# Kernel tuning notes

Hardware: AMD Instinct MI355X
Metric: run time of the kernel (lower is better)

Reference implementation:

```python
import jax, jax.numpy as jnp
import numpy as np
import math

B, S, HID = 16, 512, 768
NUM_LABELS = 9
NUM_HEADS = 4
HEAD_DIM = HID // NUM_HEADS
MAX_REL = 5
B_PERSON = 1
I_PERSON = 2
LN_EPS = 1e-5


def setup_inputs() -> dict:
    key = jax.random.key(0)
    ks = jax.random.split(key, 16)
    w = lambda k, shp: jax.random.normal(k, shp, dtype=jnp.float32) * 0.02
    return {
        "sequence_output": jax.random.normal(ks[0], (B, S, HID), dtype=jnp.float32),
        "Wq": w(ks[1], (HID, HID)), "bq": jnp.zeros((HID,), jnp.float32),
        "Wk": w(ks[2], (HID, HID)), "bk": jnp.zeros((HID,), jnp.float32),
        "Wv": w(ks[3], (HID, HID)), "bv": jnp.zeros((HID,), jnp.float32),
        "Wo": w(ks[4], (HID, HID)), "bo": jnp.zeros((HID,), jnp.float32),
        "ln_g": jnp.ones((HID,), jnp.float32), "ln_b": jnp.zeros((HID,), jnp.float32),
        "Ws": w(ks[5], (HID, NUM_LABELS)), "bs": jnp.zeros((NUM_LABELS,), jnp.float32),
        "entity_bias": w(ks[6], (NUM_LABELS,)),
    }


def _heads(x):
    # [B,S,HID] -> [B,H,S,D]
    return x.reshape(B, S, NUM_HEADS, HEAD_DIM).transpose(0, 2, 1, 3)


def reference(sequence_output, Wq, bq, Wk, bk, Wv, bv, Wo, bo, ln_g, ln_b, Ws, bs, entity_bias):
    x = sequence_output
    q = _heads(x @ Wq + bq)
    k = _heads(x @ Wk + bk)
    v = _heads(x @ Wv + bv)

    scores = jnp.einsum("bhqd,bhkd->bhqk", q, k)
    # relative position bias: exp(-0.1 * clamp(|i-j|, 0, MAX_REL)), broadcast over b,h
    idx = jnp.arange(S, dtype=jnp.float32)
    dist = jnp.abs(idx[None, :] - idx[:, None])  # [S,S]
    rel_bias = jnp.exp(-0.1 * jnp.clip(dist, 0.0, float(MAX_REL)))
    dist_mask = -0.1 * dist
    scores = (scores + rel_bias) / math.sqrt(HEAD_DIM) + dist_mask
    probs = jax.nn.softmax(scores, axis=-1)  # dropout is identity in eval

    ctx = jnp.einsum("bhqk,bhkd->bhqd", probs, v)
    ctx = ctx.transpose(0, 2, 1, 3).reshape(B, S, HID)
    out = ctx @ Wo + bo

    h = x + out
    mu = jnp.mean(h, axis=-1, keepdims=True)
    var = jnp.mean(jnp.square(h - mu), axis=-1, keepdims=True)
    h = (h - mu) * jax.lax.rsqrt(var + LN_EPS) * ln_g + ln_b

    span_logits = h @ Ws + bs  # [B,S,L]
    # vectorized entity-bias post-process: the torch loop adds entity_bias[I_PERSON]
    # TWICE to final_logits[:, j, I_PERSON] whenever argmax(span_logits[:, j-1]) == B_PERSON
    prev_is_b = jnp.argmax(span_logits[:, :-1], axis=-1) == B_PERSON  # [B,S-1]
    bump = jnp.where(prev_is_b, 2.0 * entity_bias[I_PERSON], 0.0)
    final_logits = span_logits.at[:, 1:, I_PERSON].add(bump)
    return final_logits
```

## Files before the change

kernel.cpp:

```cpp
#include <hip/hip_runtime.h>
#include <math.h>

#define SEQ 512
#define HID 768
#define NBATCH 16
#define ROWS 8192
#define INV_SQRT_D 0.07216878364870323f

typedef short s8v __attribute__((ext_vector_type(8)));
typedef _Float16 h8v __attribute__((ext_vector_type(8)));
typedef float f4v __attribute__((ext_vector_type(4)));
typedef unsigned short u16;

__device__ __forceinline__ u16 f2h(float f) {
  _Float16 h = (_Float16)f;
  return __builtin_bit_cast(u16, h);
}

__device__ __forceinline__ void llds16(const u16* g, u16* l) {
  __builtin_amdgcn_global_load_lds(
      (const __attribute__((address_space(1))) void*)g,
      (__attribute__((address_space(3))) void*)l, 16, 0, 0);
}

template <int KSTEPS>
__device__ __forceinline__ void mm_core128(
    const u16* __restrict__ A, const int lda,
    const u16* __restrict__ B, const int ldb,
    u16* lds, f4v (&acc)[4][4])
{
  const int tid = threadIdx.x;
  const int w = tid >> 6, ln = tid & 63;
  const u16* src = (w >> 1) ? B : A;
  const int ld = (w >> 1) ? ldb : lda;
  const int half = w & 1;
  const int srow = ln >> 2;
  const int csw  = ((ln & 3) - (ln >> 3)) & 3;
  const int ml = ln & 15;
  const int fo2 = (((ln >> 4) + ((ln >> 1) & 3)) & 3) * 8;
  const int wr = (w >> 1) * 64, wc = (w & 1) * 64;

  const u16* gp[4];
  u16* lp[4];
#pragma unroll
  for (int t = 0; t < 4; ++t) {
    const int row = half * 64 + t * 16 + srow;
    gp[t] = src + (size_t)row * ld + csw * 8;
    lp[t] = lds + (w >> 1) * 4096 + half * 2048 + t * 512;
  }

  for (int kp = 0; kp < KSTEPS / 2; ++kp) {
    const int k0 = kp * 64;
    __syncthreads();
#pragma unroll
    for (int t = 0; t < 4; ++t) {
      llds16(gp[t] + k0,      lp[t]);
      llds16(gp[t] + k0 + 32, lp[t] + 8192);
    }
    __syncthreads();
#pragma unroll
    for (int sub = 0; sub < 2; ++sub) {
      const int so = sub * 8192;
      h8v a[4], b[4];
#pragma unroll
      for (int i = 0; i < 4; ++i)
        a[i] = *(const h8v*)&lds[so + (wr + i * 16 + ml) * 32 + fo2];
#pragma unroll
      for (int j = 0; j < 4; ++j)
        b[j] = *(const h8v*)&lds[so + 4096 + (wc + j * 16 + ml) * 32 + fo2];
#pragma unroll
      for (int i = 0; i < 4; ++i)
#pragma unroll
        for (int j = 0; j < 4; ++j)
          acc[i][j] = __builtin_amdgcn_mfma_f32_16x16x32_f16(a[i], b[j], acc[i][j], 0, 0, 0);
    }
  }
}

__global__ __launch_bounds__(256) void splitx(const float* __restrict__ x,
                                              u16* __restrict__ xh)
{
  const int i = blockIdx.x * 256 + threadIdx.x;
  const float4 v = ((const float4*)x)[i];
  ((ushort4*)xh)[i] = make_ushort4(f2h(v.x), f2h(v.y), f2h(v.z), f2h(v.w));
}

__global__ __launch_bounds__(256) void wsplit(
    const float* __restrict__ Wq, const float* __restrict__ Wk,
    const float* __restrict__ Wv, const float* __restrict__ Wo,
    u16* __restrict__ WTh)
{
  __shared__ float t[32][33];
  const int z = blockIdx.z;
  const float* W = (z == 0) ? Wq : (z == 1) ? Wk : (z == 2) ? Wv : Wo;
  const int n0 = blockIdx.x * 32, k0 = blockIdx.y * 32;
  const int tx = threadIdx.x & 31, ty = threadIdx.x >> 5;
#pragma unroll
  for (int i = 0; i < 4; ++i)
    t[ty + 8 * i][tx] = W[(size_t)(k0 + ty + 8 * i) * HID + n0 + tx];
  __syncthreads();
#pragma unroll
  for (int i = 0; i < 4; ++i) {
    const float v = t[tx][ty + 8 * i];
    const size_t idx = (size_t)z * HID * HID + (size_t)(n0 + ty + 8 * i) * HID + k0 + tx;
    WTh[idx] = f2h(v);
  }
}

__global__ __launch_bounds__(256, 4) void qkv_mm(
    const u16* __restrict__ xh, const u16* __restrict__ WTh,
    const float* __restrict__ bq, const float* __restrict__ bk, const float* __restrict__ bv,
    u16* __restrict__ qh, u16* __restrict__ kh, u16* __restrict__ vTh)
{
  __shared__ u16 lds[18432];
  const int id = blockIdx.x;
  const int xcd = id & 7;
  const int s = id >> 3;
  const int bx = s % 6;
  const int yl = (s / 6) & 7;
  const int z  = s / 48;
  const int bm = (yl * 8 + xcd) * 128;
  const int bn = bx * 128;
  const size_t wtoff = (size_t)z * HID * HID + (size_t)bn * HID;
  f4v acc[4][4];
#pragma unroll
  for (int i = 0; i < 4; ++i)
#pragma unroll
    for (int j = 0; j < 4; ++j) acc[i][j] = (f4v)0.f;
  mm_core128<24>(xh + (size_t)bm * HID, HID, WTh + wtoff, HID, lds, acc);
  const int tid = threadIdx.x, w = tid >> 6, ln = tid & 63;
  const int ml = ln & 15, quad = ln >> 4;
  const int wr = (w >> 1) * 64, wc = (w & 1) * 64;
  if (z == 2) {
    __syncthreads();
#pragma unroll
    for (int i = 0; i < 4; ++i)
#pragma unroll
      for (int j = 0; j < 4; ++j) {
        const int ncol = wc + j * 16 + ml;
        const float bv_ = bv[bn + ncol];
#pragma unroll
        for (int r = 0; r < 4; ++r) {
          const int srow = wr + i * 16 + quad * 4 + r;
          lds[ncol * 136 + srow] = f2h(acc[i][j][r] + bv_);
        }
      }
    __syncthreads();
    u16* vb = vTh + (size_t)(bm >> 9) * HID * SEQ;
    const int sq0 = bm & 511;
    const int c8 = (tid & 15) * 8;
#pragma unroll
    for (int p = 0; p < 8; ++p) {
      const int nl = p * 16 + (tid >> 4);
      const s8v val = *(const s8v*)&lds[nl * 136 + c8];
      *(s8v*)&vb[(size_t)(bn + nl) * SEQ + sq0 + c8] = val;
    }
  } else {
    const float* bias = (z == 0) ? bq : bk;
    u16* dst = (z == 0) ? qh : kh;
    __syncthreads();
#pragma unroll
    for (int i = 0; i < 4; ++i)
#pragma unroll
      for (int j = 0; j < 4; ++j) {
        const int col = wc + j * 16 + ml;
        const float bv_ = bias[bn + col];
#pragma unroll
        for (int r = 0; r < 4; ++r) {
          const int row = wr + i * 16 + quad * 4 + r;
          lds[row * 132 + col] = f2h(acc[i][j][r] + bv_);
        }
      }
    __syncthreads();
    const int c8 = (tid & 15) * 8;
#pragma unroll
    for (int p = 0; p < 8; ++p) {
      const int rl = p * 16 + (tid >> 4);
      const s8v val = *(const s8v*)&lds[rl * 132 + c8];
      *(s8v*)&dst[(size_t)(bm + rl) * HID + bn + c8] = val;
    }
  }
}

__global__ __launch_bounds__(256, 2) void attn_fused(
    const u16* __restrict__ qh, const u16* __restrict__ kh,
    const u16* __restrict__ vTh, u16* __restrict__ ch)
{
  __shared__ u16 lds[31232];
  __shared__ float gtab[1024];
  __shared__ float red[4][32];
  const int f = blockIdx.x;
  const int xcd = f & 7, s = f >> 3;
  const int z = xcd * 8 + (s >> 3);
  const int bm = (s & 7) * 64;
  const int b = z >> 2, hh = z & 3;
  const int tid = threadIdx.x, w = tid >> 6, ln = tid & 63;
  const int ml = ln & 15, quad = ln >> 4;
  const int rh = w >> 1, ch2 = w & 1;

  for (int t = tid; t < 1023; t += 256) {
    const float fd = fabsf((float)(t - 511));
    gtab[t] = INV_SQRT_D * __expf(-0.1f * fminf(fd, 5.0f)) - 0.1f * fd;
  }

  const u16* qbase = qh + (size_t)(b * SEQ + bm + rh * 32) * HID + hh * 192;
  const u16* kbase = kh + (size_t)b * SEQ * HID + hh * 192;
  const u16* vbase = vTh + (size_t)b * HID * SEQ + (size_t)(hh * 192) * SEQ;

  h8v qf[2][6];
#pragma unroll
  for (int i = 0; i < 2; ++i)
#pragma unroll
    for (int ks = 0; ks < 6; ++ks)
      qf[i][ks] = *(const h8v*)(qbase + (size_t)(i * 16 + ml) * HID + ks * 32 + quad * 8);

  int koff[6], kldso[6], voff[6], vldso[6];
#pragma unroll
  for (int c = 0; c < 6; ++c) {
    const int cc = c * 256 + tid;
    const int krow = cc / 24, kcol = cc % 24;
    koff[c]  = krow * HID + kcol * 8;
    kldso[c] = krow * 200 + kcol * 8;
    const int vrow = cc >> 3, vcol = cc & 7;
    voff[c]  = vrow * SEQ + vcol * 8;
    vldso[c] = 12800 + vrow * 72 + vcol * 8;
  }
  s8v kc[6], vc[6];
#pragma unroll
  for (int c = 0; c < 6; ++c) {
    kc[c] = *(const s8v*)(kbase + koff[c]);
    vc[c] = *(const s8v*)(vbase + voff[c]);
  }

  f4v acc2[2][6];
#pragma unroll
  for (int i = 0; i < 2; ++i)
#pragma unroll
    for (int jj = 0; jj < 6; ++jj) acc2[i][jj] = (f4v)0.f;
  float rsum[2][4];
#pragma unroll
  for (int i = 0; i < 2; ++i)
#pragma unroll
    for (int r = 0; r < 4; ++r) rsum[i][r] = 0.f;

  for (int j = 0; j < 8; ++j) {
    __syncthreads();
#pragma unroll
    for (int c = 0; c < 6; ++c) {
      *(s8v*)&lds[kldso[c]] = kc[c];
      *(s8v*)&lds[vldso[c]] = vc[c];
    }
    __syncthreads();
    if (j < 7) {
      const int ko = (j + 1) * 64;
#pragma unroll
      for (int c = 0; c < 6; ++c) {
        kc[c] = *(const s8v*)(kbase + (size_t)ko * HID + koff[c]);
        vc[c] = *(const s8v*)(vbase + ko + voff[c]);
      }
    }
    f4v sacc[2][2];
    sacc[0][0] = (f4v)0.f; sacc[0][1] = (f4v)0.f;
    sacc[1][0] = (f4v)0.f; sacc[1][1] = (f4v)0.f;
    __builtin_amdgcn_s_setprio(1);
#pragma unroll
    for (int ks = 0; ks < 6; ++ks) {
      h8v kf0 = *(const h8v*)&lds[(ch2 * 32 + ml) * 200 + ks * 32 + quad * 8];
      h8v kf1 = *(const h8v*)&lds[(ch2 * 32 + 16 + ml) * 200 + ks * 32 + quad * 8];
      sacc[0][0] = __builtin_amdgcn_mfma_f32_16x16x32_f16(qf[0][ks], kf0, sacc[0][0], 0, 0, 0);
      sacc[1][0] = __builtin_amdgcn_mfma_f32_16x16x32_f16(qf[1][ks], kf0, sacc[1][0], 0, 0, 0);
      sacc[0][1] = __builtin_amdgcn_mfma_f32_16x16x32_f16(qf[0][ks], kf1, sacc[0][1], 0, 0, 0);
      sacc[1][1] = __builtin_amdgcn_mfma_f32_16x16x32_f16(qf[1][ks], kf1, sacc[1][1], 0, 0, 0);
    }
    __builtin_amdgcn_s_setprio(0);
#pragma unroll
    for (int i = 0; i < 2; ++i)
#pragma unroll
      for (int j2 = 0; j2 < 2; ++j2) {
        const int lcol = ch2 * 32 + j2 * 16 + ml;
        const int scolg = j * 64 + lcol;
#pragma unroll
        for (int r = 0; r < 4; ++r) {
          const int lrow = rh * 32 + i * 16 + quad * 4 + r;
          const float g = gtab[bm + lrow - scolg + 511];
          const float p = __expf(fmaf(sacc[i][j2][r], INV_SQRT_D, g));
          rsum[i][r] += p;
          lds[26624 + lrow * 72 + lcol] = f2h(p);
        }
      }
    __syncthreads();
    __builtin_amdgcn_s_setprio(1);
#pragma unroll
    for (int ks = 0; ks < 2; ++ks) {
      h8v pf[2], vf[6];
#pragma unroll
      for (int i = 0; i < 2; ++i)
        pf[i] = *(const h8v*)&lds[26624 + (rh * 32 + i * 16 + ml) * 72 + ks * 32 + quad * 8];
#pragma unroll
      for (int jj = 0; jj < 6; ++jj)
        vf[jj] = *(const h8v*)&lds[12800 + (ch2 * 96 + jj * 16 + ml) * 72 + ks * 32 + quad * 8];
#pragma unroll
      for (int i = 0; i < 2; ++i)
#pragma unroll
        for (int jj = 0; jj < 6; ++jj)
          acc2[i][jj] = __builtin_amdgcn_mfma_f32_16x16x32_f16(pf[i], vf[jj], acc2[i][jj], 0, 0, 0);
    }
    __builtin_amdgcn_s_setprio(0);
  }

#pragma unroll
  for (int i = 0; i < 2; ++i)
#pragma unroll
    for (int r = 0; r < 4; ++r) {
      float t = rsum[i][r];
#pragma unroll
      for (int o = 1; o < 16; o <<= 1) t += __shfl_xor(t, o, 64);
      rsum[i][r] = t;
    }
  if (ml == 0) {
#pragma unroll
    for (int i = 0; i < 2; ++i)
#pragma unroll
      for (int r = 0; r < 4; ++r) red[w][i * 16 + quad * 4 + r] = rsum[i][r];
  }
  __syncthreads();

#pragma unroll
  for (int i = 0; i < 2; ++i)
#pragma unroll
    for (int r = 0; r < 4; ++r) {
      const int lr = i * 16 + quad * 4 + r;
      const float is = 1.0f / (red[rh * 2][lr] + red[rh * 2 + 1][lr]);
      const int m = bm + rh * 32 + lr;
#pragma unroll
      for (int jj = 0; jj < 6; ++jj) {
        const int gcol = hh * 192 + ch2 * 96 + jj * 16 + ml;
        ch[(size_t)(b * SEQ + m) * HID + gcol] = f2h(acc2[i][jj][r] * is);
      }
    }
}

__global__ __launch_bounds__(256, 4) void proj_mm(
    const u16* __restrict__ ch, const u16* __restrict__ WTh,
    const float* __restrict__ bo, const float* __restrict__ x, float* __restrict__ h)
{
  __shared__ u16 lds[16384];
  const int id = blockIdx.x;
  const int xcd = id & 7;
  const int s = id >> 3;
  const int bx = s % 6;
  const int yl = s / 6;
  const int bm = (yl * 8 + xcd) * 128;
  const int bn = bx * 128;
  const size_t wtoff = (size_t)3 * HID * HID + (size_t)bn * HID;
  f4v acc[4][4];
#pragma unroll
  for (int i = 0; i < 4; ++i)
#pragma unroll
    for (int j = 0; j < 4; ++j) acc[i][j] = (f4v)0.f;
  mm_core128<24>(ch + (size_t)bm * HID, HID, WTh + wtoff, HID, lds, acc);
  const int tid = threadIdx.x, w = tid >> 6, ln = tid & 63;
  const int ml = ln & 15, quad = ln >> 4;
  const int wr = (w >> 1) * 64, wc = (w & 1) * 64;
#pragma unroll
  for (int i = 0; i < 4; ++i)
#pragma unroll
    for (int j = 0; j < 4; ++j) {
      const int gcol = bn + wc + j * 16 + ml;
      const float bv_ = bo[gcol];
#pragma unroll
      for (int r = 0; r < 4; ++r) {
        const int grow = bm + wr + i * 16 + quad * 4 + r;
        const size_t idx = (size_t)grow * HID + gcol;
        h[idx] = acc[i][j][r] + bv_ + x[idx];
      }
    }
}

__global__ __launch_bounds__(256) void ln_logits_kernel(
    const float* __restrict__ h, const float* __restrict__ g,
    const float* __restrict__ bta, const float* __restrict__ Ws,
    const float* __restrict__ bsv, float* __restrict__ span)
{
  const int row = blockIdx.x * 4 + (threadIdx.x >> 6);
  const int lane = threadIdx.x & 63;
  const float* hr = h + (size_t)row * HID;
  float4 v[3];
#pragma unroll
  for (int sgm = 0; sgm < 3; ++sgm) v[sgm] = ((const float4*)hr)[sgm * 64 + lane];
  float s = 0.f, sq = 0.f;
#pragma unroll
  for (int sgm = 0; sgm < 3; ++sgm) {
    s  += v[sgm].x + v[sgm].y + v[sgm].z + v[sgm].w;
    sq += v[sgm].x * v[sgm].x + v[sgm].y * v[sgm].y
        + v[sgm].z * v[sgm].z + v[sgm].w * v[sgm].w;
  }
#pragma unroll
  for (int o = 1; o < 64; o <<= 1) { s += __shfl_xor(s, o, 64); sq += __shfl_xor(sq, o, 64); }
  const float mu = s / 768.0f;
  const float rs = rsqrtf(sq / 768.0f - mu * mu + 1e-5f);
  float pl[9];
#pragma unroll
  for (int l = 0; l < 9; ++l) pl[l] = 0.f;
#pragma unroll
  for (int sgm = 0; sgm < 3; ++sgm) {
    const int c0 = sgm * 256 + lane * 4;
    const float4 gg = ((const float4*)g)[sgm * 64 + lane];
    const float4 bb = ((const float4*)bta)[sgm * 64 + lane];
    const float n0 = (v[sgm].x - mu) * rs * gg.x + bb.x;
    const float n1 = (v[sgm].y - mu) * rs * gg.y + bb.y;
    const float n2 = (v[sgm].z - mu) * rs * gg.z + bb.z;
    const float n3 = (v[sgm].w - mu) * rs * gg.w + bb.w;
    const float* w0 = Ws + (size_t)c0 * 9;
#pragma unroll
    for (int l = 0; l < 9; ++l)
      pl[l] += n0 * w0[l] + n1 * w0[9 + l] + n2 * w0[18 + l] + n3 * w0[27 + l];
  }
#pragma unroll
  for (int l = 0; l < 9; ++l)
#pragma unroll
    for (int o = 1; o < 64; o <<= 1) pl[l] += __shfl_xor(pl[l], o, 64);
  if (lane == 0) {
    float* sp = span + (size_t)row * 9;
#pragma unroll
    for (int l = 0; l < 9; ++l) sp[l] = pl[l] + bsv[l];
  }
}

__global__ __launch_bounds__(256) void bump_kernel(
    const float* __restrict__ span, const float* __restrict__ eb, float* __restrict__ out)
{
  const int idx = blockIdx.x * 256 + threadIdx.x;
  if (idx >= ROWS) return;
  const int j = idx & (SEQ - 1);
  const float* sl = span + (size_t)idx * 9;
  float v[9];
#pragma unroll
  for (int l = 0; l < 9; ++l) v[l] = sl[l];
  if (j >= 1) {
    const float* sp = sl - 9;
    float m = sp[0]; int am = 0;
#pragma unroll
    for (int l = 1; l < 9; ++l) { const float t = sp[l]; if (t > m) { m = t; am = l; } }
    if (am == 1) v[2] += 2.0f * eb[2];
  }
#pragma unroll
  for (int l = 0; l < 9; ++l) out[(size_t)idx * 9 + l] = v[l];
}

extern "C" void kernel_launch(void* const* d_in, const int* in_sizes, int n_in,
                              void* d_out, int out_size, void* d_ws, size_t ws_size,
                              hipStream_t stream)
{
  (void)in_sizes; (void)n_in; (void)out_size; (void)ws_size;
  const float* x   = (const float*)d_in[0];
  const float* Wq  = (const float*)d_in[1];
  const float* bq  = (const float*)d_in[2];
  const float* Wk  = (const float*)d_in[3];
  const float* bk  = (const float*)d_in[4];
  const float* Wv  = (const float*)d_in[5];
  const float* bv  = (const float*)d_in[6];
  const float* Wo  = (const float*)d_in[7];
  const float* bo  = (const float*)d_in[8];
  const float* lng = (const float*)d_in[9];
  const float* lnb = (const float*)d_in[10];
  const float* Ws  = (const float*)d_in[11];
  const float* bs  = (const float*)d_in[12];
  const float* eb  = (const float*)d_in[13];
  float* out = (float*)d_out;

  char* ws = (char*)d_ws;
  u16* xh  = (u16*)(ws + 0);
  u16* WTh = (u16*)(ws + 25165824);
  u16* qh  = (u16*)(ws + 34603008);
  u16* kh  = (u16*)(ws + 59768832);
  u16* vTh = (u16*)(ws + 84934656);
  float* hb = (float*)(ws + 84934656);
  float* spanb = (float*)(ws + 152043520);
  u16* ctxh = qh;

  splitx<<<dim3(1572864 / 256), 256, 0, stream>>>(x, xh);
  wsplit<<<dim3(24, 24, 4), 256, 0, stream>>>(Wq, Wk, Wv, Wo, WTh);
  qkv_mm<<<dim3(1152), 256, 0, stream>>>(xh, WTh, bq, bk, bv, qh, kh, vTh);
  attn_fused<<<dim3(512), 256, 0, stream>>>(qh, kh, vTh, ctxh);
  proj_mm<<<dim3(384), 256, 0, stream>>>(ctxh, WTh, bo, x, hb);
  ln_logits_kernel<<<dim3(ROWS / 4), 256, 0, stream>>>(hb, lng, lnb, Ws, bs, spanb);
  bump_kernel<<<dim3(ROWS / 256), 256, 0, stream>>>(spanb, eb, out);
}
```

Baseline: 201.2 us.

## Load K/V tiles directly to LDS with swizzled layout in attention kernel

Replaces the register-staged K and V tile prefetch (global load to registers, then store to LDS) with direct global_load_lds transfers into an unpadded, XOR-style swizzled LDS layout. Fragment reads use a matching swizzled offset so bank conflicts stay low without padding. This frees registers and cuts LDS footprint. The cost is the lost software prefetch overlap: loads are now issued right before the barrier each iteration rather than one tile ahead.

```diff
diff --git a/kernel.cpp b/kernel.cpp
--- a/kernel.cpp
+++ b/kernel.cpp
@@ -186,7 +186,7 @@
     const u16* __restrict__ qh, const u16* __restrict__ kh,
     const u16* __restrict__ vTh, u16* __restrict__ ch)
 {
-  __shared__ u16 lds[31232];
+  __shared__ u16 lds[29184];
   __shared__ float gtab[1024];
   __shared__ float red[4][32];
   const int f = blockIdx.x;
@@ -197,6 +197,7 @@
   const int tid = threadIdx.x, w = tid >> 6, ln = tid & 63;
   const int ml = ln & 15, quad = ln >> 4;
   const int rh = w >> 1, ch2 = w & 1;
+  const int fo2 = ((quad + ((ml >> 1) & 3)) & 3) * 8;
 
   for (int t = tid; t < 1023; t += 256) {
     const float fd = fabsf((float)(t - 511));
@@ -214,23 +215,10 @@
     for (int ks = 0; ks < 6; ++ks)
       qf[i][ks] = *(const h8v*)(qbase + (size_t)(i * 16 + ml) * HID + ks * 32 + quad * 8);
 
-  int koff[6], kldso[6], voff[6], vldso[6];
-#pragma unroll
-  for (int c = 0; c < 6; ++c) {
-    const int cc = c * 256 + tid;
-    const int krow = cc / 24, kcol = cc % 24;
-    koff[c]  = krow * HID + kcol * 8;
-    kldso[c] = krow * 200 + kcol * 8;
-    const int vrow = cc >> 3, vcol = cc & 7;
-    voff[c]  = vrow * SEQ + vcol * 8;
-    vldso[c] = 12800 + vrow * 72 + vcol * 8;
-  }
-  s8v kc[6], vc[6];
-#pragma unroll
-  for (int c = 0; c < 6; ++c) {
-    kc[c] = *(const s8v*)(kbase + koff[c]);
-    vc[c] = *(const s8v*)(vbase + voff[c]);
-  }
+  const int srow16 = ln >> 2;
+  const int csw = ((ln & 3) - (ln >> 3)) & 3;
+  const u16* ksrc = kbase + (size_t)(w * 16 + srow16) * HID + csw * 8;
+  const u16* vsrc = vbase + (size_t)(w * 48 + srow16) * SEQ + csw * 8;
 
   f4v acc2[2][6];
 #pragma unroll
@@ -246,27 +234,23 @@
   for (int j = 0; j < 8; ++j) {
     __syncthreads();
 #pragma unroll
-    for (int c = 0; c < 6; ++c) {
-      *(s8v*)&lds[kldso[c]] = kc[c];
-      *(s8v*)&lds[vldso[c]] = vc[c];
-    }
-    __syncthreads();
-    if (j < 7) {
-      const int ko = (j + 1) * 64;
-#pragma unroll
-      for (int c = 0; c < 6; ++c) {
-        kc[c] = *(const s8v*)(kbase + (size_t)ko * HID + koff[c]);
-        vc[c] = *(const s8v*)(vbase + ko + voff[c]);
-      }
-    }
+    for (int st = 0; st < 6; ++st)
+      llds16(ksrc + (size_t)(j * 64) * HID + st * 32, lds + st * 2048 + w * 512);
+#pragma unroll
+    for (int st = 0; st < 2; ++st)
+#pragma unroll
+      for (int o = 0; o < 3; ++o)
+        llds16(vsrc + (size_t)(o * 16) * SEQ + j * 64 + st * 32,
+               lds + 12288 + st * 6144 + w * 1536 + o * 512);
+    __syncthreads();
     f4v sacc[2][2];
     sacc[0][0] = (f4v)0.f; sacc[0][1] = (f4v)0.f;
     sacc[1][0] = (f4v)0.f; sacc[1][1] = (f4v)0.f;
     __builtin_amdgcn_s_setprio(1);
 #pragma unroll
     for (int ks = 0; ks < 6; ++ks) {
-      h8v kf0 = *(const h8v*)&lds[(ch2 * 32 + ml) * 200 + ks * 32 + quad * 8];
-      h8v kf1 = *(const h8v*)&lds[(ch2 * 32 + 16 + ml) * 200 + ks * 32 + quad * 8];
+      h8v kf0 = *(const h8v*)&lds[ks * 2048 + (ch2 * 32 + ml) * 32 + fo2];
+      h8v kf1 = *(const h8v*)&lds[ks * 2048 + (ch2 * 32 + 16 + ml) * 32 + fo2];
       sacc[0][0] = __builtin_amdgcn_mfma_f32_16x16x32_f16(qf[0][ks], kf0, sacc[0][0], 0, 0, 0);
       sacc[1][0] = __builtin_amdgcn_mfma_f32_16x16x32_f16(qf[1][ks], kf0, sacc[1][0], 0, 0, 0);
       sacc[0][1] = __builtin_amdgcn_mfma_f32_16x16x32_f16(qf[0][ks], kf1, sacc[0][1], 0, 0, 0);
@@ -285,7 +269,7 @@
           const float g = gtab[bm + lrow - scolg + 511];
           const float p = __expf(fmaf(sacc[i][j2][r], INV_SQRT_D, g));
           rsum[i][r] += p;
-          lds[26624 + lrow * 72 + lcol] = f2h(p);
+          lds[24576 + lrow * 72 + lcol] = f2h(p);
         }
       }
     __syncthreads();
@@ -295,10 +279,10 @@
       h8v pf[2], vf[6];
 #pragma unroll
       for (int i = 0; i < 2; ++i)
-        pf[i] = *(const h8v*)&lds[26624 + (rh * 32 + i * 16 + ml) * 72 + ks * 32 + quad * 8];
+        pf[i] = *(const h8v*)&lds[24576 + (rh * 32 + i * 16 + ml) * 72 + ks * 32 + quad * 8];
 #pragma unroll
       for (int jj = 0; jj < 6; ++jj)
-        vf[jj] = *(const h8v*)&lds[12800 + (ch2 * 96 + jj * 16 + ml) * 72 + ks * 32 + quad * 8];
+        vf[jj] = *(const h8v*)&lds[12288 + ks * 6144 + (ch2 * 96 + jj * 16 + ml) * 32 + fo2];
 #pragma unroll
       for (int i = 0; i < 2; ++i)
 #pragma unroll
```

After: 199.1 us. About the same (-1.1%).
